# Kernel optimization log

Measured on AMD Instinct MI355X. Metric: run time of the kernel, lower is better.

The kernel has to match this reference:

```python
import jax, jax.numpy as jnp
import numpy as np

N_NODES = 50000
N_EDGES = 1600000
N_INPUT = 256
HID = 32
OUT = N_INPUT // 2
EPS = 1e-12


def gcn_conv(x, edge_index, W, b):
    # Standard GCNConv: D^{-1/2} (A + I) D^{-1/2} X W + b
    N = x.shape[0]
    loop = jnp.arange(N)
    src = jnp.concatenate([edge_index[0], loop])
    dst = jnp.concatenate([edge_index[1], loop])
    deg = jax.ops.segment_sum(jnp.ones_like(src, dtype=x.dtype), dst, num_segments=N)
    dinv = jax.lax.rsqrt(jnp.maximum(deg, 1.0))  # deg >= 1 due to self-loops
    norm = dinv[src] * dinv[dst]                  # [E+N]
    h = x @ W                                     # [N, out]
    msg = h[src] * norm[:, None]                  # gather + scale
    out = jax.ops.segment_sum(msg, dst, num_segments=N)
    return out + b


def l2_normalize(z):
    n = jnp.linalg.norm(z, axis=1, keepdims=True)
    return z / jnp.maximum(n, EPS)


def setup_inputs() -> dict:
    key = jax.random.key(0)
    ks = jax.random.split(key, 9)
    x = jax.random.normal(ks[0], (N_NODES, N_INPUT), dtype=jnp.float32)
    ei_u = jax.random.randint(ks[1], (2, N_EDGES), 0, N_NODES)
    ei_u2 = jax.random.randint(ks[2], (2, N_EDGES), 0, N_NODES)
    s_in = 1.0 / np.sqrt(N_INPUT)
    s_hid = 1.0 / np.sqrt(HID)
    W_in = jax.random.normal(ks[3], (N_INPUT, HID), dtype=jnp.float32) * s_in
    b_in = jnp.zeros((HID,), dtype=jnp.float32)
    W_hid = jax.random.normal(ks[4], (HID, HID), dtype=jnp.float32) * s_hid
    b_hid = jnp.zeros((HID,), dtype=jnp.float32)
    W_out = jax.random.normal(ks[5], (HID, OUT), dtype=jnp.float32) * s_hid
    b_out = jnp.zeros((OUT,), dtype=jnp.float32)
    return {"x": x, "edge_index_u": ei_u, "edge_index_u2": ei_u2,
            "W_in": W_in, "b_in": b_in, "W_hid": W_hid, "b_hid": b_hid,
            "W_out": W_out, "b_out": b_out}


def reference(x, edge_index_u, edge_index_u2, W_in, b_in, W_hid, b_hid, W_out, b_out):
    # layer 1 on both views
    x1 = gcn_conv(x, edge_index_u, W_in, b_in)
    x2 = gcn_conv(x, edge_index_u2, W_in, b_in)
    sim = jnp.sum(l2_normalize(x1) * l2_normalize(x2), axis=1, keepdims=True)
    mian = x1 + x2 * sim
    sup = x2 + x1 * sim
    # layer 2
    x1 = gcn_conv(mian, edge_index_u, W_hid, b_hid)
    x2 = gcn_conv(sup, edge_index_u2, W_hid, b_hid)
    sim = jnp.sum(l2_normalize(x1) * l2_normalize(x2), axis=1, keepdims=True)
    mian = x1 + x2 * sim
    sup = x2 + x1 * sim
    # layer 3: note both branches use edge_index_u (as in source)
    x1 = gcn_conv(mian, edge_index_u, W_out, b_out)
    x2 = gcn_conv(sup, edge_index_u, W_out, b_out)
    return jnp.concatenate([x1, x2], axis=1)
```

## Files before the change

### kernel.cpp

```cpp
#include <hip/hip_runtime.h>
#include <hip/hip_bf16.h>

#define NN 50000
#define NE 1600000
#define NIN 256
#define HID 32
#define FOUT 128
#define OSTR 256
#define NSB ((NN + 255) / 256)
#define CHUNK 4096
#define NCH ((NE + CHUNK - 1) / CHUNK)

static constexpr float EPS = 1e-12f;

__device__ __forceinline__ float b2f(unsigned short s) {
    return __uint_as_float((unsigned)s << 16);
}
__device__ __forceinline__ unsigned short f2b(float f) {
    unsigned u = __float_as_uint(f);
    u += 0x7FFFu + ((u >> 16) & 1u);
    return (unsigned short)(u >> 16);
}
__device__ __forceinline__ unsigned pack2(float a, float b) {
    return (unsigned)f2b(a) | ((unsigned)f2b(b) << 16);
}

__global__ __launch_bounds__(256) void k_hist(const int* __restrict__ dstA,
                                              const int* __restrict__ dstB,
                                              unsigned* __restrict__ hcA,
                                              unsigned* __restrict__ hcB, int half) {
    __shared__ unsigned h[NSB];
    for (int i = threadIdx.x; i < NSB; i += 256) h[i] = 0u;
    __syncthreads();
    bool sec = blockIdx.x >= half;
    int c = sec ? blockIdx.x - half : blockIdx.x;
    const int* dst = sec ? dstB : dstA;
    unsigned* hc = sec ? hcB : hcA;
    int beg = c * CHUNK, end = min(beg + CHUNK, NE);
    for (int e = beg + (int)threadIdx.x; e < end; e += 256)
        atomicAdd(&h[dst[e] >> 8], 1u);
    __syncthreads();
    for (int i = threadIdx.x; i < NSB; i += 256) hc[(size_t)c * NSB + i] = h[i];
}

__global__ __launch_bounds__(256) void k_cscan(unsigned* __restrict__ hcA,
                                               unsigned* __restrict__ hcB,
                                               unsigned* __restrict__ totA,
                                               unsigned* __restrict__ totB, int half) {
    __shared__ unsigned tile[256];
    __shared__ unsigned carry;
    bool sec = blockIdx.x >= half;
    int sb = sec ? blockIdx.x - half : blockIdx.x;
    unsigned* hc = sec ? hcB : hcA;
    unsigned* tot = sec ? totB : totA;
    if (threadIdx.x == 0) carry = 0u;
    __syncthreads();
    for (int base = 0; base < NCH; base += 256) {
        int c = base + (int)threadIdx.x;
        unsigned v = (c < NCH) ? hc[(size_t)c * NSB + sb] : 0u;
        tile[threadIdx.x] = v;
        __syncthreads();
        for (int off = 1; off < 256; off <<= 1) {
            unsigned t = (threadIdx.x >= (unsigned)off) ? tile[threadIdx.x - off] : 0u;
            __syncthreads();
            tile[threadIdx.x] += t;
            __syncthreads();
        }
        if (c < NCH) hc[(size_t)c * NSB + sb] = carry + tile[threadIdx.x] - v;
        __syncthreads();
        if (threadIdx.x == 0) carry += tile[255];
        __syncthreads();
    }
    if (threadIdx.x == 0) tot[sb] = carry;
}

__global__ __launch_bounds__(256) void k_bscan(const unsigned* __restrict__ totA,
                                               const unsigned* __restrict__ totB,
                                               int* __restrict__ bbA, int* __restrict__ bbB) {
    __shared__ unsigned tile[256];
    const unsigned* tot = blockIdx.x ? totB : totA;
    int* bb = blockIdx.x ? bbB : bbA;
    unsigned v = (threadIdx.x < NSB) ? tot[threadIdx.x] : 0u;
    tile[threadIdx.x] = v;
    __syncthreads();
    for (int off = 1; off < 256; off <<= 1) {
        unsigned t = (threadIdx.x >= (unsigned)off) ? tile[threadIdx.x - off] : 0u;
        __syncthreads();
        tile[threadIdx.x] += t;
        __syncthreads();
    }
    if (threadIdx.x < NSB) bb[threadIdx.x] = (int)(tile[threadIdx.x] - v);
    if (threadIdx.x == 0) bb[NSB] = NE;
}

__global__ __launch_bounds__(256) void k_bin1(const int* __restrict__ srcA,
                                              const int* __restrict__ dstA,
                                              const unsigned* __restrict__ hcA,
                                              const int* __restrict__ bbA,
                                              int* __restrict__ tmpA,
                                              const int* __restrict__ srcB,
                                              const int* __restrict__ dstB,
                                              const unsigned* __restrict__ hcB,
                                              const int* __restrict__ bbB,
                                              int* __restrict__ tmpB, int half) {
    __shared__ unsigned hbase[NSB];
    __shared__ unsigned hcur[NSB];
    __shared__ unsigned hscan[NSB];
    __shared__ unsigned tile[256];
    __shared__ unsigned pay[CHUNK];
    __shared__ unsigned gpos[CHUNK];
    bool sec = blockIdx.x >= half;
    int c = sec ? blockIdx.x - half : blockIdx.x;
    const int* src = sec ? srcB : srcA;
    const int* dst = sec ? dstB : dstA;
    const unsigned* hc = sec ? hcB : hcA;
    const int* bb = sec ? bbB : bbA;
    int* tmp = sec ? tmpB : tmpA;
    for (int i = threadIdx.x; i < NSB; i += 256) {
        hbase[i] = (unsigned)bb[i] + hc[(size_t)c * NSB + i];
        hcur[i] = 0u;
    }
    __syncthreads();
    int beg = c * CHUNK;
    int len = min(CHUNK, NE - beg);
    int d[16], s[16];
#pragma unroll
    for (int j = 0; j < 16; ++j) {
        int idx = j * 256 + (int)threadIdx.x;
        if (idx < len) { d[j] = dst[beg + idx]; s[j] = src[beg + idx]; }
        else d[j] = -1;
    }
#pragma unroll
    for (int j = 0; j < 16; ++j)
        if (d[j] >= 0) atomicAdd(&hcur[d[j] >> 8], 1u);
    __syncthreads();
    unsigned v = (threadIdx.x < NSB) ? hcur[threadIdx.x] : 0u;
    tile[threadIdx.x] = v;
    __syncthreads();
    for (int off = 1; off < 256; off <<= 1) {
        unsigned t = (threadIdx.x >= (unsigned)off) ? tile[threadIdx.x - off] : 0u;
        __syncthreads();
        tile[threadIdx.x] += t;
        __syncthreads();
    }
    if (threadIdx.x < NSB) {
        unsigned excl = tile[threadIdx.x] - v;
        hscan[threadIdx.x] = excl;
        hcur[threadIdx.x] = excl;
    }
    __syncthreads();
#pragma unroll
    for (int j = 0; j < 16; ++j) {
        if (d[j] >= 0) {
            int sb = d[j] >> 8;
            unsigned p = atomicAdd(&hcur[sb], 1u);
            pay[p] = ((unsigned)(d[j] & 255) << 16) | (unsigned)s[j];
            gpos[p] = hbase[sb] + (p - hscan[sb]);
        }
    }
    __syncthreads();
    for (int i = threadIdx.x; i < len; i += 256)
        tmp[gpos[i]] = (int)pay[i];
}

__global__ __launch_bounds__(256) void k_bin2(const int* __restrict__ tmpA,
                                              const int* __restrict__ bbA,
                                              unsigned short* __restrict__ csrA,
                                              unsigned* __restrict__ degA,
                                              float* __restrict__ dinvA,
                                              int* __restrict__ rpA,
                                              const int* __restrict__ tmpB,
                                              const int* __restrict__ bbB,
                                              unsigned short* __restrict__ csrB,
                                              unsigned* __restrict__ degB,
                                              float* __restrict__ dinvB,
                                              int* __restrict__ rpB, int half) {
    __shared__ unsigned cnt[256];
    __shared__ unsigned scan[256];
    __shared__ unsigned curs[256];
    bool sec = blockIdx.x >= half;
    int sb = sec ? blockIdx.x - half : blockIdx.x;
    const int* tmp = sec ? tmpB : tmpA;
    const int* bb = sec ? bbB : bbA;
    unsigned short* csr = sec ? csrB : csrA;
    unsigned* deg = sec ? degB : degA;
    float* dinv = sec ? dinvB : dinvA;
    int* rp = sec ? rpB : rpA;
    int beg = bb[sb], end = bb[sb + 1];
    cnt[threadIdx.x] = 0u;
    __syncthreads();
    for (int e = beg + (int)threadIdx.x; e < end; e += 256)
        atomicAdd(&cnt[(tmp[e] >> 16) & 255], 1u);
    __syncthreads();
    unsigned v = cnt[threadIdx.x];
    scan[threadIdx.x] = v;
    __syncthreads();
    for (int off = 1; off < 256; off <<= 1) {
        unsigned t = (threadIdx.x >= (unsigned)off) ? scan[threadIdx.x - off] : 0u;
        __syncthreads();
        scan[threadIdx.x] += t;
        __syncthreads();
    }
    unsigned excl = scan[threadIdx.x] - v;
    int n = sb * 256 + (int)threadIdx.x;
    if (n < NN) {
        deg[n] = v;
        rp[n] = beg + (int)excl;
        dinv[n] = rsqrtf((float)(v + 1u));
    }
    curs[threadIdx.x] = (unsigned)beg + excl;
    __syncthreads();
    for (int e = beg + (int)threadIdx.x; e < end; e += 256) {
        int p = tmp[e];
        unsigned pos = atomicAdd(&curs[(p >> 16) & 255], 1u);
        csr[pos] = (unsigned short)(p & 0xFFFF);
    }
}

__global__ __launch_bounds__(256) void k_gemm_in(const float* __restrict__ x,
                                                 const float* __restrict__ W,
                                                 const float* __restrict__ dinvU,
                                                 const float* __restrict__ dinvV,
                                                 unsigned short* __restrict__ hU,
                                                 unsigned short* __restrict__ hV, int N) {
    __shared__ float xs[64][65];
    int t = threadIdx.x;
    int lane = t & 63;
    int c0 = __builtin_amdgcn_readfirstlane((t >> 6) * 8);
    int rbase = blockIdx.x * 64;
    int row = rbase + lane;
    float acc[8];
#pragma unroll
    for (int j = 0; j < 8; ++j) acc[j] = 0.f;
    int sr = t >> 2;
    int so = (t & 3) * 4;
    int grow = rbase + sr;
    const float* xrow = x + (size_t)grow * NIN;
    for (int kt = 0; kt < 4; ++kt) {
        int k0 = kt * 64;
        __syncthreads();
#pragma unroll
        for (int p = 0; p < 4; ++p) {
            int ko = so + p * 16;
            float4 v = make_float4(0.f, 0.f, 0.f, 0.f);
            if (grow < N) v = *reinterpret_cast<const float4*>(xrow + k0 + ko);
            xs[ko + 0][sr] = v.x;
            xs[ko + 1][sr] = v.y;
            xs[ko + 2][sr] = v.z;
            xs[ko + 3][sr] = v.w;
        }
        __syncthreads();
        const float* Wk = W + k0 * HID + c0;
#pragma unroll 8
        for (int k = 0; k < 64; ++k) {
            float xv = xs[k][lane];
            const float* Wr = Wk + k * HID;
#pragma unroll
            for (int j = 0; j < 8; ++j)
                acc[j] = fmaf(xv, Wr[j], acc[j]);
        }
    }
    if (row >= N) return;
    float du = dinvU[row], dw = dinvV[row];
    uint4 wu, wvv;
    wu.x = pack2(acc[0] * du, acc[1] * du); wu.y = pack2(acc[2] * du, acc[3] * du);
    wu.z = pack2(acc[4] * du, acc[5] * du); wu.w = pack2(acc[6] * du, acc[7] * du);
    wvv.x = pack2(acc[0] * dw, acc[1] * dw); wvv.y = pack2(acc[2] * dw, acc[3] * dw);
    wvv.z = pack2(acc[4] * dw, acc[5] * dw); wvv.w = pack2(acc[6] * dw, acc[7] * dw);
    *reinterpret_cast<uint4*>(hU + (size_t)row * HID + c0) = wu;
    *reinterpret_cast<uint4*>(hV + (size_t)row * HID + c0) = wvv;
}

__device__ __forceinline__ void pull_sum(const unsigned short* __restrict__ t,
                                         const unsigned short* __restrict__ csr,
                                         const int* __restrict__ rowptr,
                                         const unsigned* __restrict__ deg,
                                         float* __restrict__ out, int blk, int tid) {
    int node = blk * 32 + tid / 8;
    int q = tid % 8;
    if (node >= NN) return;
    const ushort4* h4 = reinterpret_cast<const ushort4*>(t);
    int beg = rowptr[node];
    int end = beg + (int)deg[node];
    ushort4 sv = h4[(size_t)node * 8 + q];
    float4 acc0, acc1;
    acc0.x = b2f(sv.x); acc0.y = b2f(sv.y); acc0.z = b2f(sv.z); acc0.w = b2f(sv.w);
    acc1.x = 0.f; acc1.y = 0.f; acc1.z = 0.f; acc1.w = 0.f;
    int e = beg;
    for (; e + 8 <= end; e += 8) {
        int s0 = csr[e],     s1 = csr[e + 1], s2 = csr[e + 2], s3 = csr[e + 3];
        int s4 = csr[e + 4], s5 = csr[e + 5], s6 = csr[e + 6], s7 = csr[e + 7];
        ushort4 v0 = h4[(size_t)s0 * 8 + q];
        ushort4 v1 = h4[(size_t)s1 * 8 + q];
        ushort4 v2 = h4[(size_t)s2 * 8 + q];
        ushort4 v3 = h4[(size_t)s3 * 8 + q];
        ushort4 v4 = h4[(size_t)s4 * 8 + q];
        ushort4 v5 = h4[(size_t)s5 * 8 + q];
        ushort4 v6 = h4[(size_t)s6 * 8 + q];
        ushort4 v7 = h4[(size_t)s7 * 8 + q];
        acc0.x += (b2f(v0.x) + b2f(v1.x)) + (b2f(v2.x) + b2f(v3.x));
        acc0.y += (b2f(v0.y) + b2f(v1.y)) + (b2f(v2.y) + b2f(v3.y));
        acc0.z += (b2f(v0.z) + b2f(v1.z)) + (b2f(v2.z) + b2f(v3.z));
        acc0.w += (b2f(v0.w) + b2f(v1.w)) + (b2f(v2.w) + b2f(v3.w));
        acc1.x += (b2f(v4.x) + b2f(v5.x)) + (b2f(v6.x) + b2f(v7.x));
        acc1.y += (b2f(v4.y) + b2f(v5.y)) + (b2f(v6.y) + b2f(v7.y));
        acc1.z += (b2f(v4.z) + b2f(v5.z)) + (b2f(v6.z) + b2f(v7.z));
        acc1.w += (b2f(v4.w) + b2f(v5.w)) + (b2f(v6.w) + b2f(v7.w));
    }
    if (e + 4 <= end) {
        int s0 = csr[e], s1 = csr[e + 1], s2 = csr[e + 2], s3 = csr[e + 3];
        ushort4 v0 = h4[(size_t)s0 * 8 + q];
        ushort4 v1 = h4[(size_t)s1 * 8 + q];
        ushort4 v2 = h4[(size_t)s2 * 8 + q];
        ushort4 v3 = h4[(size_t)s3 * 8 + q];
        acc1.x += (b2f(v0.x) + b2f(v1.x)) + (b2f(v2.x) + b2f(v3.x));
        acc1.y += (b2f(v0.y) + b2f(v1.y)) + (b2f(v2.y) + b2f(v3.y));
        acc1.z += (b2f(v0.z) + b2f(v1.z)) + (b2f(v2.z) + b2f(v3.z));
        acc1.w += (b2f(v0.w) + b2f(v1.w)) + (b2f(v2.w) + b2f(v3.w));
        e += 4;
    }
    for (; e < end; ++e) {
        ushort4 v0 = h4[(size_t)csr[e] * 8 + q];
        acc0.x += b2f(v0.x); acc0.y += b2f(v0.y);
        acc0.z += b2f(v0.z); acc0.w += b2f(v0.w);
    }
    float4 acc;
    acc.x = acc0.x + acc1.x; acc.y = acc0.y + acc1.y;
    acc.z = acc0.z + acc1.z; acc.w = acc0.w + acc1.w;
    *reinterpret_cast<float4*>(out + (size_t)node * HID + q * 4) = acc;
}

__global__ __launch_bounds__(256) void k_pull_pair(
    const unsigned short* __restrict__ tA, const unsigned short* __restrict__ csrA,
    const int* __restrict__ rpA, const unsigned* __restrict__ degA, float* __restrict__ outA,
    const unsigned short* __restrict__ tB, const unsigned short* __restrict__ csrB,
    const int* __restrict__ rpB, const unsigned* __restrict__ degB, float* __restrict__ outB,
    int nblk) {
    int b = blockIdx.x;
    int xcd = b & 7;
    int blk = (b >> 3) * 4 + (xcd & 3);
    if (blk >= nblk) return;
    if (xcd >= 4) pull_sum(tB, csrB, rpB, degB, outB, blk, threadIdx.x);
    else          pull_sum(tA, csrA, rpA, degA, outA, blk, threadIdx.x);
}

__global__ __launch_bounds__(256) void k_mix1(const float* __restrict__ Su,
                                              const float* __restrict__ Sv,
                                              const float* __restrict__ dinvU,
                                              const float* __restrict__ dinvV,
                                              const float* __restrict__ bias,
                                              unsigned short* __restrict__ Tu,
                                              unsigned short* __restrict__ Tv) {
    int node = blockIdx.x * 32 + (threadIdx.x >> 3);
    int q = threadIdx.x & 7;
    if (node >= NN) return;
    float4 su = *reinterpret_cast<const float4*>(Su + (size_t)node * HID + 4 * q);
    float4 sv = *reinterpret_cast<const float4*>(Sv + (size_t)node * HID + 4 * q);
    float du = dinvU[node], dw = dinvV[node];
    float a0 = fmaf(su.x, du, bias[4 * q + 0]);
    float a1 = fmaf(su.y, du, bias[4 * q + 1]);
    float a2 = fmaf(su.z, du, bias[4 * q + 2]);
    float a3 = fmaf(su.w, du, bias[4 * q + 3]);
    float b0 = fmaf(sv.x, dw, bias[4 * q + 0]);
    float b1 = fmaf(sv.y, dw, bias[4 * q + 1]);
    float b2 = fmaf(sv.z, dw, bias[4 * q + 2]);
    float b3 = fmaf(sv.w, dw, bias[4 * q + 3]);
    float n1 = a0 * a0 + a1 * a1 + a2 * a2 + a3 * a3;
    float n2 = b0 * b0 + b1 * b1 + b2 * b2 + b3 * b3;
    float dt = a0 * b0 + a1 * b1 + a2 * b2 + a3 * b3;
#pragma unroll
    for (int m = 4; m >= 1; m >>= 1) {
        n1 += __shfl_xor(n1, m);
        n2 += __shfl_xor(n2, m);
        dt += __shfl_xor(dt, m);
    }
    float sim = dt / (fmaxf(sqrtf(n1), EPS) * fmaxf(sqrtf(n2), EPS));
    uint2 mu, mv;
    mu.x = pack2((a0 + b0 * sim) * du, (a1 + b1 * sim) * du);
    mu.y = pack2((a2 + b2 * sim) * du, (a3 + b3 * sim) * du);
    mv.x = pack2((b0 + a0 * sim) * dw, (b1 + a1 * sim) * dw);
    mv.y = pack2((b2 + a2 * sim) * dw, (b3 + a3 * sim) * dw);
    *reinterpret_cast<uint2*>(Tu + (size_t)node * HID + 4 * q) = mu;
    *reinterpret_cast<uint2*>(Tv + (size_t)node * HID + 4 * q) = mv;
}

__global__ __launch_bounds__(256) void k_hid_mix_pack(const float* __restrict__ Su,
                                                      const float* __restrict__ Sv,
                                                      const float* __restrict__ W,
                                                      const float* __restrict__ bias,
                                                      const float* __restrict__ dinvU,
                                                      const float* __restrict__ dinvV,
                                                      unsigned short* __restrict__ Pa,
                                                      unsigned short* __restrict__ Pb) {
    __shared__ float Ws[HID * HID];
    __shared__ float zu[32][33];
    __shared__ float zv[32][33];
    int t = threadIdx.x;
    for (int i = t; i < HID * HID; i += 256) Ws[i] = W[i];
    int nb = blockIdx.x * 32;
    int l = t >> 3, q = t & 7;
    int node = nb + l;
    {
        float4 fu = make_float4(0.f, 0.f, 0.f, 0.f), fv = fu;
        if (node < NN) {
            fu = *reinterpret_cast<const float4*>(Su + (size_t)node * HID + 4 * q);
            fv = *reinterpret_cast<const float4*>(Sv + (size_t)node * HID + 4 * q);
        }
        zu[l][4 * q + 0] = fu.x; zu[l][4 * q + 1] = fu.y;
        zu[l][4 * q + 2] = fu.z; zu[l][4 * q + 3] = fu.w;
        zv[l][4 * q + 0] = fv.x; zv[l][4 * q + 1] = fv.y;
        zv[l][4 * q + 2] = fv.z; zv[l][4 * q + 3] = fv.w;
    }
    __syncthreads();
    if (node >= NN) return;
    float a[4] = {0.f, 0.f, 0.f, 0.f};
    float b[4] = {0.f, 0.f, 0.f, 0.f};
#pragma unroll
    for (int k = 0; k < HID; ++k) {
        float zuk = zu[l][k], zvk = zv[l][k];
        const float* Wk = Ws + k * HID + 4 * q;
#pragma unroll
        for (int j = 0; j < 4; ++j) {
            a[j] = fmaf(zuk, Wk[j], a[j]);
            b[j] = fmaf(zvk, Wk[j], b[j]);
        }
    }
    float du = dinvU[node], dw = dinvV[node];
#pragma unroll
    for (int j = 0; j < 4; ++j) {
        a[j] = fmaf(a[j], du, bias[4 * q + j]);
        b[j] = fmaf(b[j], dw, bias[4 * q + j]);
    }
    float n1 = a[0]*a[0] + a[1]*a[1] + a[2]*a[2] + a[3]*a[3];
    float n2 = b[0]*b[0] + b[1]*b[1] + b[2]*b[2] + b[3]*b[3];
    float dt = a[0]*b[0] + a[1]*b[1] + a[2]*b[2] + a[3]*b[3];
#pragma unroll
    for (int m = 4; m >= 1; m >>= 1) {
        n1 += __shfl_xor(n1, m);
        n2 += __shfl_xor(n2, m);
        dt += __shfl_xor(dt, m);
    }
    float sim = dt / (fmaxf(sqrtf(n1), EPS) * fmaxf(sqrtf(n2), EPS));
    uint2 ma, mb;
    ma.x = pack2((a[0] + b[0] * sim) * du, (a[1] + b[1] * sim) * du);
    ma.y = pack2((a[2] + b[2] * sim) * du, (a[3] + b[3] * sim) * du);
    mb.x = pack2((b[0] + a[0] * sim) * du, (b[1] + a[1] * sim) * du);
    mb.y = pack2((b[2] + a[2] * sim) * du, (b[3] + a[3] * sim) * du);
    *reinterpret_cast<uint2*>(Pa + (size_t)node * HID + 4 * q) = ma;
    *reinterpret_cast<uint2*>(Pb + (size_t)node * HID + 4 * q) = mb;
}

__global__ __launch_bounds__(512) void k_gemm_out2(const float* __restrict__ Qa,
                                                   const float* __restrict__ Qb,
                                                   const float* __restrict__ dinvU,
                                                   const float* __restrict__ W,
                                                   const float* __restrict__ b,
                                                   float* __restrict__ out, int N) {
    __shared__ float ob[32 * 257];
    int lane = threadIdx.x & 63;
    int wv = (int)(threadIdx.x >> 6);
    int view = __builtin_amdgcn_readfirstlane(wv >> 2);
    int c0 = __builtin_amdgcn_readfirstlane((wv & 3) * 32);
    int row = blockIdx.x * 64 + lane;
    bool active = row < N;
    float a[32];
#pragma unroll
    for (int j = 0; j < 32; ++j) a[j] = 0.f;
    if (active) {
        const float* Q = view ? Qb : Qa;
        const float4* q4 = reinterpret_cast<const float4*>(Q + (size_t)row * HID);
#pragma unroll 2
        for (int k4 = 0; k4 < 8; ++k4) {
            float4 v = q4[k4];
            const float* Wk = W + (k4 * 4) * FOUT + c0;
#pragma unroll
            for (int j = 0; j < 32; ++j) {
                a[j] = fmaf(v.x, Wk[j], a[j]);
                a[j] = fmaf(v.y, Wk[FOUT + j], a[j]);
                a[j] = fmaf(v.z, Wk[2 * FOUT + j], a[j]);
                a[j] = fmaf(v.w, Wk[3 * FOUT + j], a[j]);
            }
        }
    }
    float du = active ? dinvU[row] : 0.f;
    int r32 = lane & 31;
    int hl = lane >> 5;
    for (int p = 0; p < 2; ++p) {
        if (hl == p) {
            int off = r32 * 257 + view * FOUT + c0;
#pragma unroll
            for (int j = 0; j < 32; ++j)
                ob[off + j] = fmaf(a[j], du, b[c0 + j]);
        }
        __syncthreads();
        int rbase = blockIdx.x * 64 + p * 32;
        int nrows = min(32, N - rbase);
        if (nrows > 0) {
            float* obase = out + (size_t)rbase * OSTR;
            int total = nrows * OSTR;
            for (int f = threadIdx.x; f < total; f += 512)
                obase[f] = ob[f + (f >> 8)];
        }
        __syncthreads();
    }
}

extern "C" void kernel_launch(void* const* d_in, const int* in_sizes, int n_in,
                              void* d_out, int out_size, void* d_ws, size_t ws_size,
                              hipStream_t stream) {
    const float* x     = (const float*)d_in[0];
    const int*   ei_u  = (const int*)d_in[1];
    const int*   ei_u2 = (const int*)d_in[2];
    const float* W_in  = (const float*)d_in[3];
    const float* b_in  = (const float*)d_in[4];
    const float* W_hid = (const float*)d_in[5];
    const float* b_hid = (const float*)d_in[6];
    const float* W_out = (const float*)d_in[7];
    const float* b_out = (const float*)d_in[8];
    float* out = (float*)d_out;

    const int* src_u  = ei_u;
    const int* dst_u  = ei_u + NE;
    const int* src_u2 = ei_u2;
    const int* dst_u2 = ei_u2 + NE;

    char* w = (char*)d_ws;
    auto carve = [&](size_t bytes) {
        char* p = w;
        w += (bytes + 255) & ~(size_t)255;
        return p;
    };
    unsigned* hc_u   = (unsigned*)carve((size_t)NCH * NSB * sizeof(unsigned));
    unsigned* hc_u2  = (unsigned*)carve((size_t)NCH * NSB * sizeof(unsigned));
    unsigned* tot_u  = (unsigned*)carve(NSB * sizeof(unsigned));
    unsigned* tot_u2 = (unsigned*)carve(NSB * sizeof(unsigned));
    int*      bb_u   = (int*)carve((NSB + 1) * sizeof(int));
    int*      bb_u2  = (int*)carve((NSB + 1) * sizeof(int));
    unsigned* deg_u  = (unsigned*)carve(NN * sizeof(unsigned));
    unsigned* deg_u2 = (unsigned*)carve(NN * sizeof(unsigned));
    float*    dinv_u  = (float*)carve(NN * sizeof(float));
    float*    dinv_u2 = (float*)carve(NN * sizeof(float));
    int*      rp_u   = (int*)carve(NN * sizeof(int));
    int*      rp_u2  = (int*)carve(NN * sizeof(int));
    unsigned short* csr_u  = (unsigned short*)carve((size_t)NE * sizeof(unsigned short));
    unsigned short* csr_u2 = (unsigned short*)carve((size_t)NE * sizeof(unsigned short));
    unsigned short* hU = (unsigned short*)carve((size_t)NN * HID * sizeof(unsigned short));
    unsigned short* hV = (unsigned short*)carve((size_t)NN * HID * sizeof(unsigned short));
    unsigned short* Tu = (unsigned short*)carve((size_t)NN * HID * sizeof(unsigned short));
    unsigned short* Tv = (unsigned short*)carve((size_t)NN * HID * sizeof(unsigned short));
    unsigned short* Pa = (unsigned short*)carve((size_t)NN * HID * sizeof(unsigned short));
    unsigned short* Pb = (unsigned short*)carve((size_t)NN * HID * sizeof(unsigned short));
    float* Su = (float*)carve((size_t)NN * HID * sizeof(float));
    float* Sv = (float*)carve((size_t)NN * HID * sizeof(float));
    int* tmp_u  = (int*)Su;
    int* tmp_u2 = (int*)Sv;

    const int BLK = 256;
    const int gP32 = (NN + 31) / 32;
    const int nPair = ((gP32 + 3) / 4) * 8;
    const int gR64 = (NN + 63) / 64;

    k_hist<<<2 * NCH, BLK, 0, stream>>>(dst_u, dst_u2, hc_u, hc_u2, NCH);
    k_cscan<<<2 * NSB, BLK, 0, stream>>>(hc_u, hc_u2, tot_u, tot_u2, NSB);
    k_bscan<<<2, BLK, 0, stream>>>(tot_u, tot_u2, bb_u, bb_u2);
    k_bin1<<<2 * NCH, BLK, 0, stream>>>(src_u, dst_u, hc_u, bb_u, tmp_u,
                                        src_u2, dst_u2, hc_u2, bb_u2, tmp_u2, NCH);
    k_bin2<<<2 * NSB, BLK, 0, stream>>>(tmp_u, bb_u, csr_u, deg_u, dinv_u, rp_u,
                                        tmp_u2, bb_u2, csr_u2, deg_u2, dinv_u2, rp_u2, NSB);

    k_gemm_in<<<gR64, BLK, 0, stream>>>(x, W_in, dinv_u, dinv_u2, hU, hV, NN);
    k_pull_pair<<<nPair, BLK, 0, stream>>>(hU, csr_u, rp_u, deg_u, Su,
                                           hV, csr_u2, rp_u2, deg_u2, Sv, gP32);
    k_mix1<<<gP32, BLK, 0, stream>>>(Su, Sv, dinv_u, dinv_u2, b_in, Tu, Tv);

    k_pull_pair<<<nPair, BLK, 0, stream>>>(Tu, csr_u, rp_u, deg_u, Su,
                                           Tv, csr_u2, rp_u2, deg_u2, Sv, gP32);
    k_hid_mix_pack<<<gP32, BLK, 0, stream>>>(Su, Sv, W_hid, b_hid, dinv_u, dinv_u2, Pa, Pb);

    k_pull_pair<<<nPair, BLK, 0, stream>>>(Pa, csr_u, rp_u, deg_u, Su,
                                           Pb, csr_u, rp_u, deg_u, Sv, gP32);
    k_gemm_out2<<<gR64, 512, 0, stream>>>(Su, Sv, dinv_u, W_out, b_out, out, NN);

    (void)in_sizes; (void)n_in; (void)out_size; (void)ws_size;
}
```

Baseline: 204.1 us.

## Rewrite input GEMM with direct row loads and split-K across wave pairs

The input projection kernel stops staging x tiles through transposed shared memory. Each lane now loads its own row with float4 reads directly from global memory. The K dimension is split across two wave groups in a 512-thread block, and the partial sums are reduced through a small shared buffer. This removes the LDS transpose and most barriers but makes lanes read strided rows, which may reduce load coalescing.

Result: slower. 209.1 us (+2.5%).

```diff
diff --git a/kernel.cpp b/kernel.cpp
--- a/kernel.cpp
+++ b/kernel.cpp
@@ -217,50 +217,47 @@
     }
 }
 
-__global__ __launch_bounds__(256) void k_gemm_in(const float* __restrict__ x,
+__global__ __launch_bounds__(512) void k_gemm_in(const float* __restrict__ x,
                                                  const float* __restrict__ W,
                                                  const float* __restrict__ dinvU,
                                                  const float* __restrict__ dinvV,
                                                  unsigned short* __restrict__ hU,
                                                  unsigned short* __restrict__ hV, int N) {
-    __shared__ float xs[64][65];
+    __shared__ float part[4][64][9];
     int t = threadIdx.x;
     int lane = t & 63;
-    int c0 = __builtin_amdgcn_readfirstlane((t >> 6) * 8);
-    int rbase = blockIdx.x * 64;
-    int row = rbase + lane;
+    int w = t >> 6;
+    int ws = __builtin_amdgcn_readfirstlane(w & 3);
+    int kh = __builtin_amdgcn_readfirstlane(w >> 2);
+    int c0 = ws * 8;
+    int row = blockIdx.x * 64 + lane;
     float acc[8];
 #pragma unroll
     for (int j = 0; j < 8; ++j) acc[j] = 0.f;
-    int sr = t >> 2;
-    int so = (t & 3) * 4;
-    int grow = rbase + sr;
-    const float* xrow = x + (size_t)grow * NIN;
-    for (int kt = 0; kt < 4; ++kt) {
-        int k0 = kt * 64;
-        __syncthreads();
-#pragma unroll
-        for (int p = 0; p < 4; ++p) {
-            int ko = so + p * 16;
-            float4 v = make_float4(0.f, 0.f, 0.f, 0.f);
-            if (grow < N) v = *reinterpret_cast<const float4*>(xrow + k0 + ko);
-            xs[ko + 0][sr] = v.x;
-            xs[ko + 1][sr] = v.y;
-            xs[ko + 2][sr] = v.z;
-            xs[ko + 3][sr] = v.w;
-        }
-        __syncthreads();
-        const float* Wk = W + k0 * HID + c0;
-#pragma unroll 8
-        for (int k = 0; k < 64; ++k) {
-            float xv = xs[k][lane];
-            const float* Wr = Wk + k * HID;
-#pragma unroll
-            for (int j = 0; j < 8; ++j)
-                acc[j] = fmaf(xv, Wr[j], acc[j]);
-        }
-    }
-    if (row >= N) return;
+    if (row < N) {
+        const float4* xr = reinterpret_cast<const float4*>(x + (size_t)row * NIN) + kh * 32;
+        const float* Wb = W + (kh * 128) * HID + c0;
+#pragma unroll 4
+        for (int i = 0; i < 32; ++i) {
+            float4 v = xr[i];
+            const float* Wk = Wb + (i * 4) * HID;
+#pragma unroll
+            for (int j = 0; j < 8; ++j) {
+                acc[j] = fmaf(v.x, Wk[j], acc[j]);
+                acc[j] = fmaf(v.y, Wk[HID + j], acc[j]);
+                acc[j] = fmaf(v.z, Wk[2 * HID + j], acc[j]);
+                acc[j] = fmaf(v.w, Wk[3 * HID + j], acc[j]);
+            }
+        }
+    }
+    if (kh == 1) {
+#pragma unroll
+        for (int j = 0; j < 8; ++j) part[ws][lane][j] = acc[j];
+    }
+    __syncthreads();
+    if (kh == 1 || row >= N) return;
+#pragma unroll
+    for (int j = 0; j < 8; ++j) acc[j] += part[ws][lane][j];
     float du = dinvU[row], dw = dinvV[row];
     uint4 wu, wvv;
     wu.x = pack2(acc[0] * du, acc[1] * du); wu.y = pack2(acc[2] * du, acc[3] * du);
@@ -568,7 +565,7 @@
     k_bin2<<<2 * NSB, BLK, 0, stream>>>(tmp_u, bb_u, csr_u, deg_u, dinv_u, rp_u,
                                         tmp_u2, bb_u2, csr_u2, deg_u2, dinv_u2, rp_u2, NSB);
 
-    k_gemm_in<<<gR64, BLK, 0, stream>>>(x, W_in, dinv_u, dinv_u2, hU, hV, NN);
+    k_gemm_in<<<gR64, 512, 0, stream>>>(x, W_in, dinv_u, dinv_u2, hU, hV, NN);
     k_pull_pair<<<nPair, BLK, 0, stream>>>(hU, csr_u, rp_u, deg_u, Su,
                                            hV, csr_u2, rp_u2, deg_u2, Sv, gP32);
     k_mix1<<<gP32, BLK, 0, stream>>>(Su, Sv, dinv_u, dinv_u2, b_in, Tu, Tv);
```
